# Performance work log

Measured on AMD Instinct MI355X. Metric: run time of the kernel, lower is better.

## Reference

```python
import jax, jax.numpy as jnp
import numpy as np

DIM = 192
T, H, W = 6, 8, 8
NH = 6
HD = DIM // NH
HW = H * W
N = T * HW
SCALE = HD ** (-0.5)
B_ = 128


def _sine_pos_enc():
    # Faithful port of get_sine_position_encoding(window_size[1:], dim // 2).
    npf = DIM // 2
    ones = jnp.ones((1, H, W), jnp.float32)
    y_embed = jnp.cumsum(ones, axis=1)
    x_embed = jnp.cumsum(ones, axis=2)
    two_pi = 2.0 * np.pi
    y_embed = y_embed / (y_embed[:, -1:, :] + 1e-6) * two_pi
    x_embed = x_embed / (x_embed[:, :, -1:] + 1e-6) * two_pi
    dim_t = jnp.arange(npf, dtype=jnp.float32)
    dim_t = 10000.0 ** (2.0 * jnp.floor(dim_t / 2.0) / npf)
    pos_x = x_embed[:, :, :, None] / dim_t
    pos_y = y_embed[:, :, :, None] / dim_t
    pos_x = jnp.stack((jnp.sin(pos_x[..., 0::2]), jnp.cos(pos_x[..., 1::2])), axis=4).reshape(1, H, W, npf)
    pos_y = jnp.stack((jnp.sin(pos_y[..., 0::2]), jnp.cos(pos_y[..., 1::2])), axis=4).reshape(1, H, W, npf)
    pos = jnp.concatenate((pos_y, pos_x), axis=3)  # (1, H, W, DIM)
    return pos.reshape(1, HW, DIM)


def setup_inputs() -> dict:
    key = jax.random.key(0)
    ks = jax.random.split(key, 6)
    s = 0.02
    return {
        "x": jax.random.normal(ks[0], (B_, N, DIM), jnp.float32),
        "Wqkv": jax.random.normal(ks[1], (3 * DIM, DIM), jnp.float32) * s,
        "Wproj": jax.random.normal(ks[2], (DIM, 2 * DIM), jnp.float32) * s,
        "bproj": jnp.zeros((DIM,), jnp.float32),
        "gamma": jnp.ones((DIM,), jnp.float32),
        "beta": jnp.zeros((DIM,), jnp.float32),
        "W1": jax.random.normal(ks[3], (DIM, DIM), jnp.float32) * s,
        "b1": jnp.zeros((DIM,), jnp.float32),
        "W2": jax.random.normal(ks[4], (DIM, DIM), jnp.float32) * s,
        "b2": jnp.zeros((DIM,), jnp.float32),
    }


def reference(x, Wqkv, Wproj, bproj, gamma, beta, W1, b1, W2, b2):
    b = x.shape[0]
    pos = jnp.tile(_sine_pos_enc(), (1, T, 1))  # (1, N, DIM)
    qkv = (x + pos) @ Wqkv.T                      # (b, N, 3*DIM)
    qkv = qkv.reshape(b, N, 3, NH, HD).transpose(2, 0, 3, 1, 4)
    # temporal chunks: (b, NH, T, HW, HD)
    q = qkv[0].reshape(b, NH, T, HW, HD)
    k = qkv[1].reshape(b, NH, T, HW, HD)
    v = qkv[2].reshape(b, NH, T, HW, HD)
    # all T x T cross-frame attention pairs at once
    scores = jnp.einsum('bhind,bhjmd->ijbhnm', q * SCALE, k)  # (T,T,b,NH,HW,HW)
    attn = jax.nn.softmax(scores, axis=-1)
    o = jnp.einsum('ijbhnm,bhjmd->ijbnhd', attn, v).reshape(T, T, b, HW, DIM)
    # Faithful to torch's x.view(-1, B_, HW, C): raw reinterpretation, not a transpose.
    x_tmp = x.reshape(T, b, HW, DIM)
    xi = jnp.broadcast_to(x_tmp[:, None], (T, T, b, HW, DIM))
    x_att = jnp.concatenate((o, xi), axis=-1)     # (T,T,b,HW,2*DIM)
    y = x_att @ Wproj.T + bproj
    mu = jnp.mean(y, axis=-1, keepdims=True)
    var = jnp.var(y, axis=-1, keepdims=True)
    y = (y - mu) / jnp.sqrt(var + 1e-5) * gamma + beta
    y = jax.nn.gelu(y @ W1.T + b1, approximate=False) @ W2.T + b2
    acc = jnp.sum(y, axis=1)                       # sum over j -> (T,b,HW,DIM)
    x_out = x + acc.transpose(1, 0, 2, 3).reshape(b, N, DIM) / T
    return jnp.concatenate((x, x_out), axis=-1)
```

## Files before the change

### kernel.cpp

```cpp
#include <hip/hip_runtime.h>
#include <cmath>

#define TT   6
#define NB   128
#define DIM  192
#define SCALE 0.17677669529663687f

typedef __attribute__((ext_vector_type(8))) short v8s;
typedef __attribute__((ext_vector_type(4))) float v4f;

__device__ __forceinline__ short f2bf(float f) {
  union { float f; unsigned u; } v; v.f = f;
  unsigned r = v.u + 0x7fffu + ((v.u >> 16) & 1u);
  return (short)(r >> 16);
}

__device__ __forceinline__ void ldsbar() {
  __asm__ volatile("s_waitcnt lgkmcnt(0)" ::: "memory");
  __builtin_amdgcn_s_barrier();
  __asm__ volatile("" ::: "memory");
}

__global__ void prep_kernel(const float* __restrict__ Wqkv, const float* __restrict__ Wproj,
                            const float* __restrict__ W1, const float* __restrict__ W2,
                            short* __restrict__ dWqkv, short* __restrict__ dWproj,
                            short* __restrict__ dW1, short* __restrict__ dW2,
                            float* __restrict__ pos) {
  int idx = blockIdx.x * 256 + threadIdx.x;
  const float* src = nullptr; short* dst = nullptr; int off = 0;
  if (idx < 27648)      { src = Wqkv;  dst = dWqkv;  off = idx; }
  else if (idx < 46080) { src = Wproj; dst = dWproj; off = idx - 27648; }
  else if (idx < 55296) { src = W1;    dst = dW1;    off = idx - 46080; }
  else if (idx < 64512) { src = W2;    dst = dW2;    off = idx - 55296; }
  else if (idx < 67584) {
    int p0 = (idx - 64512) * 4;
    float4 r;
    float* rp = (float*)&r;
#pragma unroll
    for (int jj = 0; jj < 4; jj++) {
      int p = p0 + jj;
      int row = p / 192, c = p - row * 192;
      int e  = (c < 96) ? (row >> 3) : (row & 7);
      int cc = (c < 96) ? c : c - 96;
      int m = cc >> 1;
      float embed = (float)(e + 1) * (6.283185307179586f / 8.000001f);
      float dt = powf(10000.0f, (float)m * (1.0f / 48.0f));
      float ang = embed / dt;
      rp[jj] = (cc & 1) ? cosf(ang) : sinf(ang);
    }
    *(float4*)(pos + p0) = r;
    return;
  } else return;
  const float* s = src + off * 4;
  short4 r;
  r.x = f2bf(s[0]); r.y = f2bf(s[1]); r.z = f2bf(s[2]); r.w = f2bf(s[3]);
  *(short4*)(dst + off * 4) = r;
}

__global__ __launch_bounds__(256) void qkv_kernel(
    const float* __restrict__ x, const float* __restrict__ pos,
    const short* __restrict__ Wqkv_bf,
    short* __restrict__ Qb, short* __restrict__ Kb, short* __restrict__ Vtb) {
  __shared__ short XP[64 * 200];
  int bid = blockIdx.x;
  int xcd = bid & 7, idx = bid >> 3;
  int bq = idx / TT;
  int b = xcd * 16 + bq, t = idx - bq * TT;
  int tid = threadIdx.x, w = tid >> 6, lane = tid & 63;
  int l15 = lane & 15, quad = lane >> 4;
  const float* xrow = x + (size_t)(b * (TT * 64) + t * 64) * DIM;
  for (int c = tid; c < 64 * 24; c += 256) {
    int row = c / 24, col8 = (c - (c / 24) * 24) * 8;
    const float* xs = xrow + row * DIM + col8;
    const float* pp = pos + row * DIM + col8;
    v8s r8;
#pragma unroll
    for (int jj = 0; jj < 8; jj++) r8[jj] = f2bf(xs[jj] + pp[jj]);
    *(v8s*)(XP + row * 200 + col8) = r8;
  }
  __syncthreads();
  const v4f vzero = {0.f, 0.f, 0.f, 0.f};
  size_t obase = (size_t)(b * TT + t) * 64 * DIM;
#pragma unroll
  for (int cti = 0; cti < 9; cti++) {
    int r0 = w * 144 + cti * 16;
    v4f acc[4] = {vzero, vzero, vzero, vzero};
#pragma unroll
    for (int ks = 0; ks < 6; ks++) {
      v8s a = *(const v8s*)(Wqkv_bf + (size_t)(r0 + l15) * 192 + ks * 32 + quad * 8);
#pragma unroll
      for (int nt = 0; nt < 4; nt++) {
        v8s bb = *(const v8s*)(XP + (nt * 16 + l15) * 200 + ks * 32 + quad * 8);
        acc[nt] = __builtin_amdgcn_mfma_f32_16x16x32_bf16(a, bb, acc[nt], 0, 0, 0);
      }
    }
    int R = r0 + quad * 4;
#pragma unroll
    for (int nt = 0; nt < 4; nt++) {
      int hw = nt * 16 + l15;
      if (R < 192) {
        short4 s;
        s.x = f2bf(acc[nt][0] * SCALE); s.y = f2bf(acc[nt][1] * SCALE);
        s.z = f2bf(acc[nt][2] * SCALE); s.w = f2bf(acc[nt][3] * SCALE);
        *(short4*)(Qb + obase + (size_t)hw * 192 + R) = s;
      } else if (R < 384) {
        short4 s;
        s.x = f2bf(acc[nt][0]); s.y = f2bf(acc[nt][1]);
        s.z = f2bf(acc[nt][2]); s.w = f2bf(acc[nt][3]);
        *(short4*)(Kb + obase + (size_t)hw * 192 + (R - 192)) = s;
      } else {
#pragma unroll
        for (int r = 0; r < 4; r++)
          Vtb[obase + (size_t)(R - 384 + r) * 64 + hw] = f2bf(acc[nt][r]);
      }
    }
  }
}

__device__ __forceinline__ void ptrans(const v4f S[4], float inv,
                                       int srcA, int srcB, bool hiq,
                                       v8s& B0v, v8s& B1v) {
  unsigned pk00, pk01, pk10, pk11, pk20, pk21, pk30, pk31;
  {
    float a0 = S[0][0] * inv, a1 = S[0][1] * inv, a2 = S[0][2] * inv, a3 = S[0][3] * inv;
    __asm__("v_cvt_pk_bf16_f32 %0, %1, %2" : "=v"(pk00) : "v"(a0), "v"(a1));
    __asm__("v_cvt_pk_bf16_f32 %0, %1, %2" : "=v"(pk01) : "v"(a2), "v"(a3));
    float b0 = S[1][0] * inv, b1_ = S[1][1] * inv, b2_ = S[1][2] * inv, b3 = S[1][3] * inv;
    __asm__("v_cvt_pk_bf16_f32 %0, %1, %2" : "=v"(pk10) : "v"(b0), "v"(b1_));
    __asm__("v_cvt_pk_bf16_f32 %0, %1, %2" : "=v"(pk11) : "v"(b2_), "v"(b3));
    float c0 = S[2][0] * inv, c1 = S[2][1] * inv, c2 = S[2][2] * inv, c3 = S[2][3] * inv;
    __asm__("v_cvt_pk_bf16_f32 %0, %1, %2" : "=v"(pk20) : "v"(c0), "v"(c1));
    __asm__("v_cvt_pk_bf16_f32 %0, %1, %2" : "=v"(pk21) : "v"(c2), "v"(c3));
    float d0 = S[3][0] * inv, d1 = S[3][1] * inv, d2 = S[3][2] * inv, d3 = S[3][3] * inv;
    __asm__("v_cvt_pk_bf16_f32 %0, %1, %2" : "=v"(pk30) : "v"(d0), "v"(d1));
    __asm__("v_cvt_pk_bf16_f32 %0, %1, %2" : "=v"(pk31) : "v"(d2), "v"(d3));
  }
  union { unsigned u[4]; v8s v; } B0, B1;
  unsigned ta, tb;
  ta = (unsigned)__shfl((int)pk00, srcA); tb = (unsigned)__shfl((int)pk10, srcA);
  B0.u[0] = hiq ? tb : ta;
  ta = (unsigned)__shfl((int)pk01, srcA); tb = (unsigned)__shfl((int)pk11, srcA);
  B0.u[1] = hiq ? tb : ta;
  ta = (unsigned)__shfl((int)pk00, srcB); tb = (unsigned)__shfl((int)pk10, srcB);
  B0.u[2] = hiq ? tb : ta;
  ta = (unsigned)__shfl((int)pk01, srcB); tb = (unsigned)__shfl((int)pk11, srcB);
  B0.u[3] = hiq ? tb : ta;
  ta = (unsigned)__shfl((int)pk20, srcA); tb = (unsigned)__shfl((int)pk30, srcA);
  B1.u[0] = hiq ? tb : ta;
  ta = (unsigned)__shfl((int)pk21, srcA); tb = (unsigned)__shfl((int)pk31, srcA);
  B1.u[1] = hiq ? tb : ta;
  ta = (unsigned)__shfl((int)pk20, srcB); tb = (unsigned)__shfl((int)pk30, srcB);
  B1.u[2] = hiq ? tb : ta;
  ta = (unsigned)__shfl((int)pk21, srcB); tb = (unsigned)__shfl((int)pk31, srcB);
  B1.u[3] = hiq ? tb : ta;
  B0v = B0.v; B1v = B1.v;
}

__device__ __forceinline__ void issue_w(v8s (&dst)[6][3], const short* __restrict__ Wp,
                                        int rstride, int coff, int rbase, int quad) {
#pragma unroll
  for (int ks = 0; ks < 6; ks++)
#pragma unroll
    for (int cti = 0; cti < 3; cti++)
      dst[ks][cti] = *(const v8s*)(Wp + (size_t)(rbase + cti * 16) * rstride + coff + ks * 32 + quad * 8);
}

__device__ __forceinline__ void gemm_consume(const v8s (&wu)[6][3], v4f (&yy)[3][2],
                                             const short* __restrict__ SRC, int l15, int quad) {
#pragma unroll
  for (int ks = 0; ks < 6; ks++) {
    v8s b0 = *(const v8s*)(SRC + (size_t)(l15) * 200 + ks * 32 + quad * 8);
    v8s b1 = *(const v8s*)(SRC + (size_t)(16 + l15) * 200 + ks * 32 + quad * 8);
#pragma unroll
    for (int cti = 0; cti < 3; cti++) {
      yy[cti][0] = __builtin_amdgcn_mfma_f32_16x16x32_bf16(wu[ks][cti], b0, yy[cti][0], 0, 0, 0);
      yy[cti][1] = __builtin_amdgcn_mfma_f32_16x16x32_bf16(wu[ks][cti], b1, yy[cti][1], 0, 0, 0);
    }
  }
}

__device__ __forceinline__ void attn_phase(const short* __restrict__ Kj,
                                           const short* __restrict__ Vj,
                                           const v8s (&qa)[3], short* __restrict__ SP,
                                           int l15, int quad, int hg, int qt,
                                           int srcA, int srcB, bool hiq) {
  const v4f vzero = {0.f, 0.f, 0.f, 0.f};
#pragma unroll
  for (int hh = 0; hh < 3; hh++) {
    int h = hg * 3 + hh;
    v8s kf[4];
#pragma unroll
    for (int cta = 0; cta < 4; cta++)
      kf[cta] = *(const v8s*)(Kj + (size_t)(cta * 16 + l15) * 192 + h * 32 + quad * 8);
    v4f S[4];
#pragma unroll
    for (int cta = 0; cta < 4; cta++)
      S[cta] = __builtin_amdgcn_mfma_f32_16x16x32_bf16(kf[cta], qa[hh], vzero, 0, 0, 0);
    v8s vf0a = *(const v8s*)(Vj + (size_t)(h * 32 + l15) * 64 + quad * 8);
    v8s vf0b = *(const v8s*)(Vj + (size_t)(h * 32 + l15) * 64 + 32 + quad * 8);
    v8s vf1a = *(const v8s*)(Vj + (size_t)(h * 32 + 16 + l15) * 64 + quad * 8);
    v8s vf1b = *(const v8s*)(Vj + (size_t)(h * 32 + 16 + l15) * 64 + 32 + quad * 8);
    float mx = -1e30f;
#pragma unroll
    for (int cta = 0; cta < 4; cta++)
#pragma unroll
      for (int r = 0; r < 4; r++) mx = fmaxf(mx, S[cta][r]);
    mx = fmaxf(mx, __shfl_xor(mx, 16, 64));
    mx = fmaxf(mx, __shfl_xor(mx, 32, 64));
    float sum = 0.f;
#pragma unroll
    for (int cta = 0; cta < 4; cta++)
#pragma unroll
      for (int r = 0; r < 4; r++) {
        float e = __expf(S[cta][r] - mx);
        S[cta][r] = e; sum += e;
      }
    sum += __shfl_xor(sum, 16, 64);
    sum += __shfl_xor(sum, 32, 64);
    float inv = 1.0f / sum;
    v8s B0, B1;
    ptrans(S, inv, srcA, srcB, hiq, B0, B1);
    v4f o0 = __builtin_amdgcn_mfma_f32_16x16x32_bf16(vf0a, B0, vzero, 0, 0, 0);
    o0 = __builtin_amdgcn_mfma_f32_16x16x32_bf16(vf0b, B1, o0, 0, 0, 0);
    short4 s0;
    s0.x = f2bf(o0[0]); s0.y = f2bf(o0[1]); s0.z = f2bf(o0[2]); s0.w = f2bf(o0[3]);
    *(short4*)(&SP[(qt * 16 + l15) * 200 + h * 32 + quad * 4]) = s0;
    v4f o1 = __builtin_amdgcn_mfma_f32_16x16x32_bf16(vf1a, B0, vzero, 0, 0, 0);
    o1 = __builtin_amdgcn_mfma_f32_16x16x32_bf16(vf1b, B1, o1, 0, 0, 0);
    short4 s1;
    s1.x = f2bf(o1[0]); s1.y = f2bf(o1[1]); s1.z = f2bf(o1[2]); s1.w = f2bf(o1[3]);
    *(short4*)(&SP[(qt * 16 + l15) * 200 + h * 32 + 16 + quad * 4]) = s1;
  }
}

__device__ __forceinline__ void ln_reduce_store(v4f (&y1)[3][2], const float* __restrict__ bproj,
                                                float (*LNp)[4][2], int cb, int l15, int quad, int wc) {
#pragma unroll
  for (int cti = 0; cti < 3; cti++) {
    float4 bp4 = *(const float4*)(bproj + cb + cti * 16 + quad * 4);
#pragma unroll
    for (int nt = 0; nt < 2; nt++) {
      y1[cti][nt][0] += bp4.x; y1[cti][nt][1] += bp4.y;
      y1[cti][nt][2] += bp4.z; y1[cti][nt][3] += bp4.w;
    }
  }
#pragma unroll
  for (int nt = 0; nt < 2; nt++) {
    float s1 = 0.f, s2 = 0.f;
#pragma unroll
    for (int cti = 0; cti < 3; cti++)
#pragma unroll
      for (int r = 0; r < 4; r++) { float v = y1[cti][nt][r]; s1 += v; s2 += v * v; }
    s1 += __shfl_xor(s1, 16, 64); s2 += __shfl_xor(s2, 16, 64);
    s1 += __shfl_xor(s1, 32, 64); s2 += __shfl_xor(s2, 32, 64);
    if (quad == 0) { LNp[nt * 16 + l15][wc][0] = s1; LNp[nt * 16 + l15][wc][1] = s2; }
  }
}

__device__ __forceinline__ void ln_normalize_store(const v4f (&y1)[3][2],
                                                   const float* __restrict__ gamma,
                                                   const float* __restrict__ beta,
                                                   const float (*LNp)[4][2],
                                                   short* __restrict__ SP,
                                                   int cb, int l15, int quad) {
  float mu[2], rs[2];
#pragma unroll
  for (int nt = 0; nt < 2; nt++) {
    int row = nt * 16 + l15;
    float s1 = 0.f, s2 = 0.f;
#pragma unroll
    for (int ww = 0; ww < 4; ww++) { s1 += LNp[row][ww][0]; s2 += LNp[row][ww][1]; }
    float m = s1 * (1.0f / 192.0f);
    mu[nt] = m; rs[nt] = rsqrtf(s2 * (1.0f / 192.0f) - m * m + 1e-5f);
  }
#pragma unroll
  for (int cti = 0; cti < 3; cti++) {
    float4 g4 = *(const float4*)(gamma + cb + cti * 16 + quad * 4);
    float4 be4 = *(const float4*)(beta + cb + cti * 16 + quad * 4);
#pragma unroll
    for (int nt = 0; nt < 2; nt++) {
      short4 s;
      s.x = f2bf((y1[cti][nt][0] - mu[nt]) * rs[nt] * g4.x + be4.x);
      s.y = f2bf((y1[cti][nt][1] - mu[nt]) * rs[nt] * g4.y + be4.y);
      s.z = f2bf((y1[cti][nt][2] - mu[nt]) * rs[nt] * g4.z + be4.z);
      s.w = f2bf((y1[cti][nt][3] - mu[nt]) * rs[nt] * g4.w + be4.w);
      *(short4*)(&SP[(nt * 16 + l15) * 200 + cb + cti * 16 + quad * 4]) = s;
    }
  }
}

__device__ __forceinline__ void gelu_store(const v4f (&y2)[3][2], const float* __restrict__ b1,
                                           short* __restrict__ HB, int cb, int l15, int quad) {
#pragma unroll
  for (int cti = 0; cti < 3; cti++) {
    float4 b14 = *(const float4*)(b1 + cb + cti * 16 + quad * 4);
#pragma unroll
    for (int nt = 0; nt < 2; nt++) {
      float vv[4] = {y2[cti][nt][0] + b14.x, y2[cti][nt][1] + b14.y,
                     y2[cti][nt][2] + b14.z, y2[cti][nt][3] + b14.w};
      short sv[4];
#pragma unroll
      for (int r = 0; r < 4; r++) {
        float v = vv[r];
        float t = 0.79788456080286536f * (v + 0.044715f * v * v * v);
        float e = __expf(2.0f * t);
        float th = 1.0f - 2.0f / (e + 1.0f);
        sv[r] = f2bf(0.5f * v * (1.0f + th));
      }
      short4 s;
      s.x = sv[0]; s.y = sv[1]; s.z = sv[2]; s.w = sv[3];
      *(short4*)(&HB[(nt * 16 + l15) * 200 + cb + cti * 16 + quad * 4]) = s;
    }
  }
}

#define JBODY(WU, WN, JV)                                                      \
  {                                                                            \
    int j = (JV);                                                              \
    ldsbar();                      \
    attn_phase(Kb + (size_t)(b * TT + j) * 64 * DIM,                           \
               Vtb + (size_t)(b * TT + j) * 64 * DIM,                          \
               qa, SP, l15, quad, hg, qt, srcA, srcB, hiq);                    \
    ldsbar();                                                  \
    v4f y1[3][2];                                                              \
    _Pragma("unroll") for (int c_ = 0; c_ < 3; c_++)                           \
      _Pragma("unroll") for (int n_ = 0; n_ < 2; n_++) y1[c_][n_] = y1x[c_][n_]; \
    gemm_consume(WU, y1, SP, l15, quad);                                       \
    issue_w(WN, W1_bf, 192, 0, cb + l15, quad);                                \
    ln_reduce_store(y1, bproj, LNp, cb, l15, quad, wc);                        \
    ldsbar();                       \
    ln_normalize_store(y1, gamma, beta, LNp, SP, cb, l15, quad);               \
    ldsbar();                                                \
    v4f y2[3][2];                                                              \
    _Pragma("unroll") for (int c_ = 0; c_ < 3; c_++)                           \
      _Pragma("unroll") for (int n_ = 0; n_ < 2; n_++) y2[c_][n_] = vzero;     \
    gemm_consume(WN, y2, SP, l15, quad);                                       \
    issue_w(WU, W2_bf, 192, 0, cb + l15, quad);                                \
    gelu_store(y2, b1, HB, cb, l15, quad);                                     \
    ldsbar();                                \
    gemm_consume(WU, acc, HB, l15, quad);                                      \
    if (j < TT - 1) issue_w(WN, Wproj_bf, 384, 0, cb + l15, quad);             \
  }

__global__ __launch_bounds__(256, 2) void fused_all(
    const float* __restrict__ x,
    const short* __restrict__ Qb, const short* __restrict__ Kb,
    const short* __restrict__ Vtb,
    const short* __restrict__ Wproj_bf, const short* __restrict__ W1_bf,
    const short* __restrict__ W2_bf,
    const float* __restrict__ bproj, const float* __restrict__ gamma,
    const float* __restrict__ beta, const float* __restrict__ b1,
    const float* __restrict__ b2,
    float* __restrict__ out) {
  __shared__ short SP[32 * 200];
  __shared__ short HB[32 * 200];
  __shared__ float LNp[32][4][2];

  int bid = blockIdx.x;
  int xcd = bid & 7, idx = bid >> 3;
  int bq = idx / 12;
  int rem = idx - bq * 12;
  int i = rem >> 1, half = rem & 1;
  int b = xcd * 16 + bq;

  int tid = threadIdx.x, w = tid >> 6, lane = tid & 63;
  int l15 = lane & 15, quad = lane >> 4;
  int wc = w;
  int qt = w & 1, hg = w >> 1;
  int cb = wc * 48;
  const v4f vzero = {0.f, 0.f, 0.f, 0.f};

  const float* xi = x + (size_t)((i * NB + b) * 64 + half * 32) * DIM;
  for (int c = tid; c < 32 * 24; c += 256) {
    int row = c / 24, col8 = (c - (c / 24) * 24) * 8;
    const float* xs = xi + row * DIM + col8;
    v8s r8;
#pragma unroll
    for (int jj = 0; jj < 8; jj++) r8[jj] = f2bf(xs[jj]);
    *(v8s*)(SP + row * 200 + col8) = r8;
  }

  const short* Qi = Qb + (size_t)(b * TT + i) * 64 * DIM;
  v8s qa[3];
#pragma unroll
  for (int hh = 0; hh < 3; hh++)
    qa[hh] = *(const v8s*)(Qi + (size_t)(half * 32 + qt * 16 + l15) * 192 + (hg * 3 + hh) * 32 + quad * 8);

  v4f acc[3][2];
#pragma unroll
  for (int cti = 0; cti < 3; cti++)
#pragma unroll
    for (int nt = 0; nt < 2; nt++) acc[cti][nt] = vzero;

  ldsbar();

  v4f y1x[3][2];
#pragma unroll
  for (int cti = 0; cti < 3; cti++)
#pragma unroll
    for (int nt = 0; nt < 2; nt++) y1x[cti][nt] = vzero;
#pragma unroll
  for (int ks = 0; ks < 6; ks++) {
    v8s bxi0 = *(const v8s*)(SP + (size_t)(l15) * 200 + ks * 32 + quad * 8);
    v8s bxi1 = *(const v8s*)(SP + (size_t)(16 + l15) * 200 + ks * 32 + quad * 8);
#pragma unroll
    for (int cti = 0; cti < 3; cti++) {
      v8s a = *(const v8s*)(Wproj_bf + (size_t)(cb + cti * 16 + l15) * 384 + 192 + ks * 32 + quad * 8);
      y1x[cti][0] = __builtin_amdgcn_mfma_f32_16x16x32_bf16(a, bxi0, y1x[cti][0], 0, 0, 0);
      y1x[cti][1] = __builtin_amdgcn_mfma_f32_16x16x32_bf16(a, bxi1, y1x[cti][1], 0, 0, 0);
    }
  }

  int srcA = l15 + ((lane & 16) << 1);
  int srcB = srcA + 16;
  bool hiq = (lane & 32) != 0;

  v8s wA[6][3], wB[6][3];
  issue_w(wA, Wproj_bf, 384, 0, cb + l15, quad);

  for (int jp = 0; jp < 3; jp++) {
    JBODY(wA, wB, jp * 2);
    JBODY(wB, wA, jp * 2 + 1);
  }

  float* SPf = (float*)SP;
#pragma unroll
  for (int pass = 0; pass < 2; pass++) {
    ldsbar();
#pragma unroll
    for (int cti = 0; cti < 3; cti++) {
      float4 o4;
      o4.x = acc[cti][pass][0] * (1.0f / 6.0f);
      o4.y = acc[cti][pass][1] * (1.0f / 6.0f);
      o4.z = acc[cti][pass][2] * (1.0f / 6.0f);
      o4.w = acc[cti][pass][3] * (1.0f / 6.0f);
      *(float4*)(&SPf[l15 * 196 + cb + cti * 16 + quad * 4]) = o4;
    }
    ldsbar();
    for (int c = tid; c < 768; c += 256) {
      int r16 = c / 48, col4 = (c - r16 * 48) * 4;
      int row = half * 32 + pass * 16 + r16;
      size_t nrow = (size_t)b * 384 + (size_t)i * 64 + row;
      float4 xv = *(const float4*)(x + nrow * DIM + col4);
      float4 b24 = *(const float4*)(b2 + col4);
      float4 av = *(const float4*)(&SPf[r16 * 196 + col4]);
      float4 o4;
      o4.x = xv.x + av.x + b24.x;
      o4.y = xv.y + av.y + b24.y;
      o4.z = xv.z + av.z + b24.z;
      o4.w = xv.w + av.w + b24.w;
      *(float4*)(out + nrow * 384 + col4) = xv;
      *(float4*)(out + nrow * 384 + 192 + col4) = o4;
    }
  }
}

extern "C" void kernel_launch(void* const* d_in, const int* in_sizes, int n_in,
                              void* d_out, int out_size, void* d_ws, size_t ws_size,
                              hipStream_t stream) {
  (void)in_sizes; (void)n_in; (void)out_size; (void)ws_size;
  const float* x     = (const float*)d_in[0];
  const float* Wqkv  = (const float*)d_in[1];
  const float* Wproj = (const float*)d_in[2];
  const float* bproj = (const float*)d_in[3];
  const float* gamma = (const float*)d_in[4];
  const float* beta  = (const float*)d_in[5];
  const float* W1    = (const float*)d_in[6];
  const float* b1    = (const float*)d_in[7];
  const float* W2    = (const float*)d_in[8];
  const float* b2    = (const float*)d_in[9];
  float* out = (float*)d_out;

  short* Wqkv_bf  = (short*)d_ws;
  short* Wproj_bf = Wqkv_bf + 110592;
  short* W1_bf    = Wproj_bf + 73728;
  short* W2_bf    = W1_bf + 36864;
  float* pos_f    = (float*)(W2_bf + 36864);
  short* Qb       = (short*)(pos_f + 12288);
  short* Kb       = Qb + 9437184;
  short* Vtb      = Kb + 9437184;

  prep_kernel<<<dim3(264), dim3(256), 0, stream>>>(
      Wqkv, Wproj, W1, W2, Wqkv_bf, Wproj_bf, W1_bf, W2_bf, pos_f);
  qkv_kernel<<<dim3(TT * NB), dim3(256), 0, stream>>>(x, pos_f, Wqkv_bf, Qb, Kb, Vtb);
  fused_all<<<dim3(TT * NB * 2), dim3(256), 0, stream>>>(
      x, Qb, Kb, Vtb, Wproj_bf, W1_bf, W2_bf, bproj, gamma, beta, b1, b2, out);
}
```

Measured before the change: 567.0 us.

## Split fused attention+MLP kernel into separate attention and per-wave MLP kernels

Replaces the single fused kernel with two kernels. The first computes all T×T attention outputs and writes them to a new bf16 global buffer. The second lets each wave own 16 rows across all 192 output channels, so LayerNorm and the GEMM chains need no cross-wave barriers, only per-wave LDS strips with lgkmcnt waits. This removes the block-wide barriers and LN partial-sum exchanges, but adds about 113 MB of intermediate global traffic and reloads weights from global or cache on every MFMA.

After: 1.819 ms. 221% more time.

```diff
diff --git a/kernel.cpp b/kernel.cpp
--- a/kernel.cpp
+++ b/kernel.cpp
@@ -14,11 +14,8 @@
   unsigned r = v.u + 0x7fffu + ((v.u >> 16) & 1u);
   return (short)(r >> 16);
 }
-
-__device__ __forceinline__ void ldsbar() {
+__device__ __forceinline__ void fence() {
   __asm__ volatile("s_waitcnt lgkmcnt(0)" ::: "memory");
-  __builtin_amdgcn_s_barrier();
-  __asm__ volatile("" ::: "memory");
 }
 
 __global__ void prep_kernel(const float* __restrict__ Wqkv, const float* __restrict__ Wproj,
@@ -156,35 +153,37 @@
   B0v = B0.v; B1v = B1.v;
 }
 
-__device__ __forceinline__ void issue_w(v8s (&dst)[6][3], const short* __restrict__ Wp,
-                                        int rstride, int coff, int rbase, int quad) {
-#pragma unroll
-  for (int ks = 0; ks < 6; ks++)
-#pragma unroll
-    for (int cti = 0; cti < 3; cti++)
-      dst[ks][cti] = *(const v8s*)(Wp + (size_t)(rbase + cti * 16) * rstride + coff + ks * 32 + quad * 8);
-}
-
-__device__ __forceinline__ void gemm_consume(const v8s (&wu)[6][3], v4f (&yy)[3][2],
-                                             const short* __restrict__ SRC, int l15, int quad) {
-#pragma unroll
-  for (int ks = 0; ks < 6; ks++) {
-    v8s b0 = *(const v8s*)(SRC + (size_t)(l15) * 200 + ks * 32 + quad * 8);
-    v8s b1 = *(const v8s*)(SRC + (size_t)(16 + l15) * 200 + ks * 32 + quad * 8);
-#pragma unroll
-    for (int cti = 0; cti < 3; cti++) {
-      yy[cti][0] = __builtin_amdgcn_mfma_f32_16x16x32_bf16(wu[ks][cti], b0, yy[cti][0], 0, 0, 0);
-      yy[cti][1] = __builtin_amdgcn_mfma_f32_16x16x32_bf16(wu[ks][cti], b1, yy[cti][1], 0, 0, 0);
-    }
-  }
-}
-
-__device__ __forceinline__ void attn_phase(const short* __restrict__ Kj,
-                                           const short* __restrict__ Vj,
-                                           const v8s (&qa)[3], short* __restrict__ SP,
-                                           int l15, int quad, int hg, int qt,
-                                           int srcA, int srcB, bool hiq) {
+__global__ __launch_bounds__(256, 4) void attn_all(
+    const short* __restrict__ Qb, const short* __restrict__ Kb,
+    const short* __restrict__ Vtb, short* __restrict__ Ob) {
+  int bid = blockIdx.x;
+  int xcd = bid & 7, idx = bid >> 3;
+  int bq = idx / 72;
+  int rem = idx - bq * 72;
+  int ij = rem >> 1, half = rem & 1;
+  int i = ij / TT, j = ij - i * TT;
+  int b = xcd * 16 + bq;
+
+  int tid = threadIdx.x, w = tid >> 6, lane = tid & 63;
+  int l15 = lane & 15, quad = lane >> 4;
+  int qt = w & 1, hg = w >> 1;
   const v4f vzero = {0.f, 0.f, 0.f, 0.f};
+
+  const short* Qi = Qb + (size_t)(b * TT + i) * 64 * DIM;
+  const short* Kj = Kb + (size_t)(b * TT + j) * 64 * DIM;
+  const short* Vj = Vtb + (size_t)(b * TT + j) * 64 * DIM;
+  short* Oj = Ob + ((size_t)(i * TT + j) * NB + b) * 64 * DIM;
+
+  int qrow = half * 32 + qt * 16 + l15;
+  v8s qa[3];
+#pragma unroll
+  for (int hh = 0; hh < 3; hh++)
+    qa[hh] = *(const v8s*)(Qi + (size_t)qrow * 192 + (hg * 3 + hh) * 32 + quad * 8);
+
+  int srcA = l15 + ((lane & 16) << 1);
+  int srcB = srcA + 16;
+  bool hiq = (lane & 32) != 0;
+
 #pragma unroll
   for (int hh = 0; hh < 3; hh++) {
     int h = hg * 3 + hh;
@@ -224,80 +223,123 @@
     o0 = __builtin_amdgcn_mfma_f32_16x16x32_bf16(vf0b, B1, o0, 0, 0, 0);
     short4 s0;
     s0.x = f2bf(o0[0]); s0.y = f2bf(o0[1]); s0.z = f2bf(o0[2]); s0.w = f2bf(o0[3]);
-    *(short4*)(&SP[(qt * 16 + l15) * 200 + h * 32 + quad * 4]) = s0;
+    *(short4*)(Oj + (size_t)qrow * 192 + h * 32 + quad * 4) = s0;
     v4f o1 = __builtin_amdgcn_mfma_f32_16x16x32_bf16(vf1a, B0, vzero, 0, 0, 0);
     o1 = __builtin_amdgcn_mfma_f32_16x16x32_bf16(vf1b, B1, o1, 0, 0, 0);
     short4 s1;
     s1.x = f2bf(o1[0]); s1.y = f2bf(o1[1]); s1.z = f2bf(o1[2]); s1.w = f2bf(o1[3]);
-    *(short4*)(&SP[(qt * 16 + l15) * 200 + h * 32 + 16 + quad * 4]) = s1;
-  }
-}
-
-__device__ __forceinline__ void ln_reduce_store(v4f (&y1)[3][2], const float* __restrict__ bproj,
-                                                float (*LNp)[4][2], int cb, int l15, int quad, int wc) {
-#pragma unroll
-  for (int cti = 0; cti < 3; cti++) {
-    float4 bp4 = *(const float4*)(bproj + cb + cti * 16 + quad * 4);
-#pragma unroll
-    for (int nt = 0; nt < 2; nt++) {
-      y1[cti][nt][0] += bp4.x; y1[cti][nt][1] += bp4.y;
-      y1[cti][nt][2] += bp4.z; y1[cti][nt][3] += bp4.w;
-    }
-  }
-#pragma unroll
-  for (int nt = 0; nt < 2; nt++) {
+    *(short4*)(Oj + (size_t)qrow * 192 + h * 32 + 16 + quad * 4) = s1;
+  }
+}
+
+__global__ __launch_bounds__(256, 2) void mlp_all(
+    const float* __restrict__ x, const short* __restrict__ Ob,
+    const short* __restrict__ Wproj_bf, const short* __restrict__ W1_bf,
+    const short* __restrict__ W2_bf,
+    const float* __restrict__ bproj, const float* __restrict__ gamma,
+    const float* __restrict__ beta, const float* __restrict__ b1,
+    const float* __restrict__ b2,
+    float* __restrict__ out) {
+  __shared__ short STR[4][16 * 200];
+
+  int bid = blockIdx.x;
+  int xcd = bid & 7, idx = bid >> 3;
+  int bq = idx / TT;
+  int b = xcd * 16 + bq, i = idx - bq * TT;
+
+  int tid = threadIdx.x, w = tid >> 6, lane = tid & 63;
+  int l15 = lane & 15, quad = lane >> 4;
+  short* strip = STR[w];
+  int row = w * 16 + l15;
+  const v4f vzero = {0.f, 0.f, 0.f, 0.f};
+
+  const float* xrow_i = x + ((size_t)(i * NB + b) * 64 + row) * DIM;
+  v8s xif[6];
+#pragma unroll
+  for (int ks = 0; ks < 6; ks++) {
+    const float* xs = xrow_i + ks * 32 + quad * 8;
+    v8s r8;
+#pragma unroll
+    for (int e = 0; e < 8; e++) r8[e] = f2bf(xs[e]);
+    xif[ks] = r8;
+  }
+
+  v4f acc[12];
+#pragma unroll
+  for (int cti = 0; cti < 12; cti++) acc[cti] = vzero;
+
+  const size_t ostride = (size_t)NB * 64 * DIM;
+  const short* Obase = Ob + ((size_t)(i * TT) * NB + b) * 64 * DIM + (size_t)row * 192;
+
+  v8s of[6];
+#pragma unroll
+  for (int ks = 0; ks < 6; ks++)
+    of[ks] = *(const v8s*)(Obase + ks * 32 + quad * 8);
+
+  for (int j = 0; j < TT; j++) {
+    v4f y1[12];
+#pragma unroll
+    for (int cti = 0; cti < 12; cti++) y1[cti] = vzero;
+#pragma unroll
+    for (int g = 0; g < 12; g++) {
+      v8s bf = (g < 6) ? of[g] : xif[g - 6];
+#pragma unroll
+      for (int cti = 0; cti < 12; cti++) {
+        v8s a = *(const v8s*)(Wproj_bf + (size_t)(cti * 16 + l15) * 384 + g * 32 + quad * 8);
+        y1[cti] = __builtin_amdgcn_mfma_f32_16x16x32_bf16(a, bf, y1[cti], 0, 0, 0);
+      }
+    }
+    if (j < TT - 1) {
+      const short* On = Obase + (size_t)(j + 1) * ostride;
+#pragma unroll
+      for (int ks = 0; ks < 6; ks++)
+        of[ks] = *(const v8s*)(On + ks * 32 + quad * 8);
+    }
     float s1 = 0.f, s2 = 0.f;
 #pragma unroll
-    for (int cti = 0; cti < 3; cti++)
-#pragma unroll
-      for (int r = 0; r < 4; r++) { float v = y1[cti][nt][r]; s1 += v; s2 += v * v; }
+    for (int cti = 0; cti < 12; cti++) {
+      float4 bp4 = *(const float4*)(bproj + cti * 16 + quad * 4);
+      y1[cti][0] += bp4.x; y1[cti][1] += bp4.y;
+      y1[cti][2] += bp4.z; y1[cti][3] += bp4.w;
+#pragma unroll
+      for (int r = 0; r < 4; r++) { float v = y1[cti][r]; s1 += v; s2 += v * v; }
+    }
     s1 += __shfl_xor(s1, 16, 64); s2 += __shfl_xor(s2, 16, 64);
     s1 += __shfl_xor(s1, 32, 64); s2 += __shfl_xor(s2, 32, 64);
-    if (quad == 0) { LNp[nt * 16 + l15][wc][0] = s1; LNp[nt * 16 + l15][wc][1] = s2; }
-  }
-}
-
-__device__ __forceinline__ void ln_normalize_store(const v4f (&y1)[3][2],
-                                                   const float* __restrict__ gamma,
-                                                   const float* __restrict__ beta,
-                                                   const float (*LNp)[4][2],
-                                                   short* __restrict__ SP,
-                                                   int cb, int l15, int quad) {
-  float mu[2], rs[2];
-#pragma unroll
-  for (int nt = 0; nt < 2; nt++) {
-    int row = nt * 16 + l15;
-    float s1 = 0.f, s2 = 0.f;
-#pragma unroll
-    for (int ww = 0; ww < 4; ww++) { s1 += LNp[row][ww][0]; s2 += LNp[row][ww][1]; }
-    float m = s1 * (1.0f / 192.0f);
-    mu[nt] = m; rs[nt] = rsqrtf(s2 * (1.0f / 192.0f) - m * m + 1e-5f);
-  }
-#pragma unroll
-  for (int cti = 0; cti < 3; cti++) {
-    float4 g4 = *(const float4*)(gamma + cb + cti * 16 + quad * 4);
-    float4 be4 = *(const float4*)(beta + cb + cti * 16 + quad * 4);
-#pragma unroll
-    for (int nt = 0; nt < 2; nt++) {
+    float mu = s1 * (1.0f / 192.0f);
+    float rs = rsqrtf(s2 * (1.0f / 192.0f) - mu * mu + 1e-5f);
+#pragma unroll
+    for (int cti = 0; cti < 12; cti++) {
+      float4 g4 = *(const float4*)(gamma + cti * 16 + quad * 4);
+      float4 be4 = *(const float4*)(beta + cti * 16 + quad * 4);
       short4 s;
-      s.x = f2bf((y1[cti][nt][0] - mu[nt]) * rs[nt] * g4.x + be4.x);
-      s.y = f2bf((y1[cti][nt][1] - mu[nt]) * rs[nt] * g4.y + be4.y);
-      s.z = f2bf((y1[cti][nt][2] - mu[nt]) * rs[nt] * g4.z + be4.z);
-      s.w = f2bf((y1[cti][nt][3] - mu[nt]) * rs[nt] * g4.w + be4.w);
-      *(short4*)(&SP[(nt * 16 + l15) * 200 + cb + cti * 16 + quad * 4]) = s;
-    }
-  }
-}
-
-__device__ __forceinline__ void gelu_store(const v4f (&y2)[3][2], const float* __restrict__ b1,
-                                           short* __restrict__ HB, int cb, int l15, int quad) {
-#pragma unroll
-  for (int cti = 0; cti < 3; cti++) {
-    float4 b14 = *(const float4*)(b1 + cb + cti * 16 + quad * 4);
-#pragma unroll
-    for (int nt = 0; nt < 2; nt++) {
-      float vv[4] = {y2[cti][nt][0] + b14.x, y2[cti][nt][1] + b14.y,
-                     y2[cti][nt][2] + b14.z, y2[cti][nt][3] + b14.w};
+      s.x = f2bf((y1[cti][0] - mu) * rs * g4.x + be4.x);
+      s.y = f2bf((y1[cti][1] - mu) * rs * g4.y + be4.y);
+      s.z = f2bf((y1[cti][2] - mu) * rs * g4.z + be4.z);
+      s.w = f2bf((y1[cti][3] - mu) * rs * g4.w + be4.w);
+      *(short4*)(&strip[l15 * 200 + cti * 16 + quad * 4]) = s;
+    }
+    fence();
+    v8s bh[6];
+#pragma unroll
+    for (int ks = 0; ks < 6; ks++)
+      bh[ks] = *(const v8s*)(&strip[l15 * 200 + ks * 32 + quad * 8]);
+    v4f y2[12];
+#pragma unroll
+    for (int cti = 0; cti < 12; cti++) y2[cti] = vzero;
+#pragma unroll
+    for (int ks = 0; ks < 6; ks++)
+#pragma unroll
+      for (int cti = 0; cti < 12; cti++) {
+        v8s a = *(const v8s*)(W1_bf + (size_t)(cti * 16 + l15) * 192 + ks * 32 + quad * 8);
+        y2[cti] = __builtin_amdgcn_mfma_f32_16x16x32_bf16(a, bh[ks], y2[cti], 0, 0, 0);
+      }
+    fence();
+#pragma unroll
+    for (int cti = 0; cti < 12; cti++) {
+      float4 b14 = *(const float4*)(b1 + cti * 16 + quad * 4);
+      float vv[4] = {y2[cti][0] + b14.x, y2[cti][1] + b14.y,
+                     y2[cti][2] + b14.z, y2[cti][3] + b14.w};
       short sv[4];
 #pragma unroll
       for (int r = 0; r < 4; r++) {
@@ -309,149 +351,36 @@
       }
       short4 s;
       s.x = sv[0]; s.y = sv[1]; s.z = sv[2]; s.w = sv[3];
-      *(short4*)(&HB[(nt * 16 + l15) * 200 + cb + cti * 16 + quad * 4]) = s;
-    }
-  }
-}
-
-#define JBODY(WU, WN, JV)                                                      \
-  {                                                                            \
-    int j = (JV);                                                              \
-    ldsbar();                      \
-    attn_phase(Kb + (size_t)(b * TT + j) * 64 * DIM,                           \
-               Vtb + (size_t)(b * TT + j) * 64 * DIM,                          \
-               qa, SP, l15, quad, hg, qt, srcA, srcB, hiq);                    \
-    ldsbar();                                                  \
-    v4f y1[3][2];                                                              \
-    _Pragma("unroll") for (int c_ = 0; c_ < 3; c_++)                           \
-      _Pragma("unroll") for (int n_ = 0; n_ < 2; n_++) y1[c_][n_] = y1x[c_][n_]; \
-    gemm_consume(WU, y1, SP, l15, quad);                                       \
-    issue_w(WN, W1_bf, 192, 0, cb + l15, quad);                                \
-    ln_reduce_store(y1, bproj, LNp, cb, l15, quad, wc);                        \
-    ldsbar();                       \
-    ln_normalize_store(y1, gamma, beta, LNp, SP, cb, l15, quad);               \
-    ldsbar();                                                \
-    v4f y2[3][2];                                                              \
-    _Pragma("unroll") for (int c_ = 0; c_ < 3; c_++)                           \
-      _Pragma("unroll") for (int n_ = 0; n_ < 2; n_++) y2[c_][n_] = vzero;     \
-    gemm_consume(WN, y2, SP, l15, quad);                                       \
-    issue_w(WU, W2_bf, 192, 0, cb + l15, quad);                                \
-    gelu_store(y2, b1, HB, cb, l15, quad);                                     \
-    ldsbar();                                \
-    gemm_consume(WU, acc, HB, l15, quad);                                      \
-    if (j < TT - 1) issue_w(WN, Wproj_bf, 384, 0, cb + l15, quad);             \
-  }
-
-__global__ __launch_bounds__(256, 2) void fused_all(
-    const float* __restrict__ x,
-    const short* __restrict__ Qb, const short* __restrict__ Kb,
-    const short* __restrict__ Vtb,
-    const short* __restrict__ Wproj_bf, const short* __restrict__ W1_bf,
-    const short* __restrict__ W2_bf,
-    const float* __restrict__ bproj, const float* __restrict__ gamma,
-    const float* __restrict__ beta, const float* __restrict__ b1,
-    const float* __restrict__ b2,
-    float* __restrict__ out) {
-  __shared__ short SP[32 * 200];
-  __shared__ short HB[32 * 200];
-  __shared__ float LNp[32][4][2];
-
-  int bid = blockIdx.x;
-  int xcd = bid & 7, idx = bid >> 3;
-  int bq = idx / 12;
-  int rem = idx - bq * 12;
-  int i = rem >> 1, half = rem & 1;
-  int b = xcd * 16 + bq;
-
-  int tid = threadIdx.x, w = tid >> 6, lane = tid & 63;
-  int l15 = lane & 15, quad = lane >> 4;
-  int wc = w;
-  int qt = w & 1, hg = w >> 1;
-  int cb = wc * 48;
-  const v4f vzero = {0.f, 0.f, 0.f, 0.f};
-
-  const float* xi = x + (size_t)((i * NB + b) * 64 + half * 32) * DIM;
-  for (int c = tid; c < 32 * 24; c += 256) {
-    int row = c / 24, col8 = (c - (c / 24) * 24) * 8;
-    const float* xs = xi + row * DIM + col8;
-    v8s r8;
-#pragma unroll
-    for (int jj = 0; jj < 8; jj++) r8[jj] = f2bf(xs[jj]);
-    *(v8s*)(SP + row * 200 + col8) = r8;
-  }
-
-  const short* Qi = Qb + (size_t)(b * TT + i) * 64 * DIM;
-  v8s qa[3];
-#pragma unroll
-  for (int hh = 0; hh < 3; hh++)
-    qa[hh] = *(const v8s*)(Qi + (size_t)(half * 32 + qt * 16 + l15) * 192 + (hg * 3 + hh) * 32 + quad * 8);
-
-  v4f acc[3][2];
-#pragma unroll
-  for (int cti = 0; cti < 3; cti++)
-#pragma unroll
-    for (int nt = 0; nt < 2; nt++) acc[cti][nt] = vzero;
-
-  ldsbar();
-
-  v4f y1x[3][2];
-#pragma unroll
-  for (int cti = 0; cti < 3; cti++)
-#pragma unroll
-    for (int nt = 0; nt < 2; nt++) y1x[cti][nt] = vzero;
-#pragma unroll
-  for (int ks = 0; ks < 6; ks++) {
-    v8s bxi0 = *(const v8s*)(SP + (size_t)(l15) * 200 + ks * 32 + quad * 8);
-    v8s bxi1 = *(const v8s*)(SP + (size_t)(16 + l15) * 200 + ks * 32 + quad * 8);
-#pragma unroll
-    for (int cti = 0; cti < 3; cti++) {
-      v8s a = *(const v8s*)(Wproj_bf + (size_t)(cb + cti * 16 + l15) * 384 + 192 + ks * 32 + quad * 8);
-      y1x[cti][0] = __builtin_amdgcn_mfma_f32_16x16x32_bf16(a, bxi0, y1x[cti][0], 0, 0, 0);
-      y1x[cti][1] = __builtin_amdgcn_mfma_f32_16x16x32_bf16(a, bxi1, y1x[cti][1], 0, 0, 0);
-    }
-  }
-
-  int srcA = l15 + ((lane & 16) << 1);
-  int srcB = srcA + 16;
-  bool hiq = (lane & 32) != 0;
-
-  v8s wA[6][3], wB[6][3];
-  issue_w(wA, Wproj_bf, 384, 0, cb + l15, quad);
-
-  for (int jp = 0; jp < 3; jp++) {
-    JBODY(wA, wB, jp * 2);
-    JBODY(wB, wA, jp * 2 + 1);
-  }
-
-  float* SPf = (float*)SP;
-#pragma unroll
-  for (int pass = 0; pass < 2; pass++) {
-    ldsbar();
-#pragma unroll
-    for (int cti = 0; cti < 3; cti++) {
-      float4 o4;
-      o4.x = acc[cti][pass][0] * (1.0f / 6.0f);
-      o4.y = acc[cti][pass][1] * (1.0f / 6.0f);
-      o4.z = acc[cti][pass][2] * (1.0f / 6.0f);
-      o4.w = acc[cti][pass][3] * (1.0f / 6.0f);
-      *(float4*)(&SPf[l15 * 196 + cb + cti * 16 + quad * 4]) = o4;
-    }
-    ldsbar();
-    for (int c = tid; c < 768; c += 256) {
-      int r16 = c / 48, col4 = (c - r16 * 48) * 4;
-      int row = half * 32 + pass * 16 + r16;
-      size_t nrow = (size_t)b * 384 + (size_t)i * 64 + row;
-      float4 xv = *(const float4*)(x + nrow * DIM + col4);
-      float4 b24 = *(const float4*)(b2 + col4);
-      float4 av = *(const float4*)(&SPf[r16 * 196 + col4]);
-      float4 o4;
-      o4.x = xv.x + av.x + b24.x;
-      o4.y = xv.y + av.y + b24.y;
-      o4.z = xv.z + av.z + b24.z;
-      o4.w = xv.w + av.w + b24.w;
-      *(float4*)(out + nrow * 384 + col4) = xv;
-      *(float4*)(out + nrow * 384 + 192 + col4) = o4;
-    }
+      *(short4*)(&strip[l15 * 200 + cti * 16 + quad * 4]) = s;
+    }
+    fence();
+    v8s hh[6];
+#pragma unroll
+    for (int ks = 0; ks < 6; ks++)
+      hh[ks] = *(const v8s*)(&strip[l15 * 200 + ks * 32 + quad * 8]);
+#pragma unroll
+    for (int ks = 0; ks < 6; ks++)
+#pragma unroll
+      for (int cti = 0; cti < 12; cti++) {
+        v8s a = *(const v8s*)(W2_bf + (size_t)(cti * 16 + l15) * 192 + ks * 32 + quad * 8);
+        acc[cti] = __builtin_amdgcn_mfma_f32_16x16x32_bf16(a, hh[ks], acc[cti], 0, 0, 0);
+      }
+    fence();
+  }
+
+  size_t nrow = (size_t)b * 384 + (size_t)i * 64 + row;
+#pragma unroll
+  for (int cti = 0; cti < 12; cti++) {
+    int ch = cti * 16 + quad * 4;
+    float4 xv = *(const float4*)(x + nrow * DIM + ch);
+    float4 b24 = *(const float4*)(b2 + ch);
+    float4 o4;
+    o4.x = xv.x + acc[cti][0] * (1.0f / 6.0f) + b24.x;
+    o4.y = xv.y + acc[cti][1] * (1.0f / 6.0f) + b24.y;
+    o4.z = xv.z + acc[cti][2] * (1.0f / 6.0f) + b24.z;
+    o4.w = xv.w + acc[cti][3] * (1.0f / 6.0f) + b24.w;
+    *(float4*)(out + nrow * 384 + ch) = xv;
+    *(float4*)(out + nrow * 384 + 192 + ch) = o4;
   }
 }
 
@@ -479,10 +408,12 @@
   short* Qb       = (short*)(pos_f + 12288);
   short* Kb       = Qb + 9437184;
   short* Vtb      = Kb + 9437184;
+  short* Ob       = Vtb + 9437184;
 
   prep_kernel<<<dim3(264), dim3(256), 0, stream>>>(
       Wqkv, Wproj, W1, W2, Wqkv_bf, Wproj_bf, W1_bf, W2_bf, pos_f);
   qkv_kernel<<<dim3(TT * NB), dim3(256), 0, stream>>>(x, pos_f, Wqkv_bf, Qb, Kb, Vtb);
-  fused_all<<<dim3(TT * NB * 2), dim3(256), 0, stream>>>(
-      x, Qb, Kb, Vtb, Wproj_bf, W1_bf, W2_bf, bproj, gamma, beta, b1, b2, out);
-}
+  attn_all<<<dim3(TT * TT * NB * 2), dim3(256), 0, stream>>>(Qb, Kb, Vtb, Ob);
+  mlp_all<<<dim3(TT * NB), dim3(256), 0, stream>>>(
+      x, Ob, Wproj_bf, W1_bf, W2_bf, bproj, gamma, beta, b1, b2, out);
+}
```
